# Kernel optimization log

Measured on AMD Instinct MI355X. Metric: run time of the kernel, lower is better.

## Reference

```python
import jax, jax.numpy as jnp
import numpy as np

TAU = 0.4
EPS = 1e-8


def setup_inputs() -> dict:
    key = jax.random.key(0)
    k1, k2 = jax.random.split(key)
    B, N, C, M = 4, 4096, 256, 2048
    l_feat = jax.random.normal(k1, (B, N, C), dtype=jnp.float32)
    g_feat = jax.random.normal(k2, (B, C, M), dtype=jnp.float32)
    return {"l_feat": l_feat, "g_feat": g_feat}


def reference(l_feat, g_feat):
    # l_feat: [B, N, C], g_feat: [B, C, M]
    # cosine similarity over channel dim C (torch CosineSimilarity, dim=2)
    l_norm = jnp.linalg.norm(l_feat, axis=2)          # [B, N]
    g_norm = jnp.linalg.norm(g_feat, axis=1)          # [B, M]
    dot = jnp.einsum('bnc,bcm->bnm', l_feat, g_feat)  # [B, N, M]
    cos_sim = dot / jnp.maximum(l_norm[:, :, None] * g_norm[:, None, :], EPS)
    sim = jnp.exp(cos_sim / TAU)                      # [B, N, M]
    # diag_embed(rowsum) followed by linalg.inv and bmm is exactly
    # row-wise division by the degree (row sum)
    sim = sim / jnp.sum(sim, axis=2, keepdims=True)
    # bmm(sim, g_feat^T): [B,N,M] x [B,M,C] -> [B,N,C]
    g_enh = jnp.einsum('bnm,bcm->bnc', sim, g_feat)
    return l_feat + g_enh
```

## Files before the change

kernel.cpp:

```cpp
#include <hip/hip_runtime.h>

#define B_ 4
#define N_ 4096
#define C_ 256
#define M_ 2048

typedef __attribute__((ext_vector_type(8))) short short8;
typedef __attribute__((ext_vector_type(4))) float f32x4;

union U16x8 { uint4 u4; unsigned short us[8]; short8 s8; };

__device__ __forceinline__ float bf2f(unsigned short h) {
    unsigned int u = ((unsigned int)h) << 16;
    return __builtin_bit_cast(float, u);
}
__device__ __forceinline__ unsigned short f2bf(float f) {
    unsigned int u = __builtin_bit_cast(unsigned int, f);
    u += 0x7FFFu + ((u >> 16) & 1u);
    return (unsigned short)(u >> 16);
}

#define GLB_AS(p) ((const __attribute__((address_space(1))) unsigned int*)(p))
#define LDS_AS(p) ((__attribute__((address_space(3))) unsigned int*)(p))

__global__ __launch_bounds__(256) void k_prep3(const float* __restrict__ g,
                                               unsigned short* __restrict__ gcm,
                                               unsigned short* __restrict__ gmc) {
    __shared__ float4 red4[16][16];
    __shared__ float4 sInv4[16];
    __shared__ unsigned short T[256 * 66];
    const int b = blockIdx.y, m0 = blockIdx.x * 64;
    const int tid = threadIdx.x;
    const int ml2 = tid & 15, cg = tid >> 4;
    const float* gb = g + (size_t)b * C_ * M_ + m0 + ml2 * 4;
    float4 v4[16];
    float4 ss = {0.f, 0.f, 0.f, 0.f};
#pragma unroll
    for (int i = 0; i < 16; ++i) {
        v4[i] = *(const float4*)(gb + (size_t)(cg * 16 + i) * M_);
        ss.x += v4[i].x * v4[i].x; ss.y += v4[i].y * v4[i].y;
        ss.z += v4[i].z * v4[i].z; ss.w += v4[i].w * v4[i].w;
    }
    red4[cg][ml2] = ss;
    __syncthreads();
    if (tid < 16) {
        float4 t = {0.f, 0.f, 0.f, 0.f};
#pragma unroll
        for (int j = 0; j < 16; ++j) {
            float4 r = red4[j][tid];
            t.x += r.x; t.y += r.y; t.z += r.z; t.w += r.w;
        }
        float4 iv;
        iv.x = 1.f / fmaxf(sqrtf(t.x), 1e-8f);
        iv.y = 1.f / fmaxf(sqrtf(t.y), 1e-8f);
        iv.z = 1.f / fmaxf(sqrtf(t.z), 1e-8f);
        iv.w = 1.f / fmaxf(sqrtf(t.w), 1e-8f);
        sInv4[tid] = iv;
    }
    __syncthreads();
    const float4 iv = sInv4[ml2];
    unsigned short* gcmb = gcm + (size_t)b * C_ * M_ + m0 + ml2 * 4;
#pragma unroll
    for (int i = 0; i < 16; ++i) {
        int c = cg * 16 + i;
        uint2 pk;
        pk.x = (unsigned)f2bf(v4[i].x) | ((unsigned)f2bf(v4[i].y) << 16);
        pk.y = (unsigned)f2bf(v4[i].z) | ((unsigned)f2bf(v4[i].w) << 16);
        *(uint2*)(gcmb + (size_t)c * M_) = pk;
        T[c * 66 + ml2 * 4 + 0] = f2bf(v4[i].x * iv.x);
        T[c * 66 + ml2 * 4 + 1] = f2bf(v4[i].y * iv.y);
        T[c * 66 + ml2 * 4 + 2] = f2bf(v4[i].z * iv.z);
        T[c * 66 + ml2 * 4 + 3] = f2bf(v4[i].w * iv.w);
    }
    __syncthreads();
    unsigned short* gmcb = gmc + ((size_t)b * M_ + m0) * C_;
#pragma unroll
    for (int j = 0; j < 8; ++j) {
        int id = j * 256 + tid;
        int mr = id >> 5, cc8 = (id & 31) * 8;
        U16x8 t;
#pragma unroll
        for (int k = 0; k < 8; ++k) t.us[k] = T[(cc8 + k) * 66 + mr];
        *(uint4*)(gmcb + (size_t)mr * C_ + cc8) = t.u4;
    }
}

__global__ __launch_bounds__(256, 2) void k_main(
    const float* __restrict__ l,
    const unsigned short* __restrict__ gcm,
    const unsigned short* __restrict__ gmc,
    float* __restrict__ out)
{
    __shared__ __align__(16) unsigned short sGmc[64 * 256];
    __shared__ __align__(16) unsigned short sGcm[256 * 64];
    __shared__ __align__(16) unsigned short sP[64 * 72];
    __shared__ float sDen[128];

    const int tid = threadIdx.x;
    const int w = tid >> 6;
    const int lane = tid & 63;
    const int l15 = lane & 15;
    const int quad = lane >> 4;
    const int b = blockIdx.y;
    const int row0 = blockIdx.x * 64;
    const int qrow0 = (w & 1) * 32;
    const int kh = w >> 1;

    int goffA[8], goffB[8];
#pragma unroll
    for (int i = 0; i < 8; ++i) {
        int p = (w * 8 + i) * 64 + lane;
        int rA = p >> 5;
        goffA[i] = rA * 256 + (((p & 31) ^ (rA & 31)) << 3);
        int rB = p >> 3;
        goffB[i] = rB * 2048 + (((p & 7) ^ (rB & 7)) << 3);
    }

    const unsigned short* gmc_b = gmc + (size_t)b * M_ * C_;
    const unsigned short* gcm_b = gcm + (size_t)b * C_ * M_;

    auto dmaA = [&](int m0) {
#pragma unroll
        for (int i = 0; i < 8; ++i)
            __builtin_amdgcn_global_load_lds(GLB_AS(gmc_b + (size_t)m0 * 256 + goffA[i]),
                                             LDS_AS(&sGmc[(w * 8 + i) * 512]), 16, 0, 0);
    };
    auto dmaB = [&](int m0) {
#pragma unroll
        for (int i = 0; i < 8; ++i)
            __builtin_amdgcn_global_load_lds(GLB_AS(gcm_b + (size_t)m0 + goffB[i]),
                                             LDS_AS(&sGcm[(w * 8 + i) * 512]), 16, 0, 0);
    };

    dmaA(0);
    dmaB(0);

    short8 qf[2][8];
#pragma unroll
    for (int rt = 0; rt < 2; ++rt) {
        const float* lrow = l + ((size_t)b * N_ + row0 + qrow0 + rt * 16 + l15) * C_;
        U16x8 qt[8];
        float ss = 0.f;
#pragma unroll
        for (int kk = 0; kk < 8; ++kk) {
            float4 x0 = *(const float4*)(lrow + kk * 32 + quad * 8);
            float4 x1 = *(const float4*)(lrow + kk * 32 + quad * 8 + 4);
            ss += x0.x*x0.x + x0.y*x0.y + x0.z*x0.z + x0.w*x0.w;
            ss += x1.x*x1.x + x1.y*x1.y + x1.z*x1.z + x1.w*x1.w;
            qt[kk].us[0] = f2bf(x0.x); qt[kk].us[1] = f2bf(x0.y);
            qt[kk].us[2] = f2bf(x0.z); qt[kk].us[3] = f2bf(x0.w);
            qt[kk].us[4] = f2bf(x1.x); qt[kk].us[5] = f2bf(x1.y);
            qt[kk].us[6] = f2bf(x1.z); qt[kk].us[7] = f2bf(x1.w);
        }
        ss += __shfl_xor(ss, 16);
        ss += __shfl_xor(ss, 32);
        const float invl = 1.0f / fmaxf(sqrtf(ss), 1e-8f);
#pragma unroll
        for (int kk = 0; kk < 8; ++kk) {
            U16x8 t;
#pragma unroll
            for (int j = 0; j < 8; ++j) t.us[j] = f2bf(bf2f(qt[kk].us[j]) * invl);
            qf[rt][kk] = t.s8;
        }
    }

    __syncthreads();

    f32x4 zero = {0.f, 0.f, 0.f, 0.f};
    f32x4 o[4][4];
#pragma unroll
    for (int i = 0; i < 4; ++i)
#pragma unroll
        for (int j = 0; j < 4; ++j) o[i][j] = zero;
    float dl[2][4] = {{0.f,0.f,0.f,0.f},{0.f,0.f,0.f,0.f}};

    for (int mt = 0; mt < 32; ++mt) {
        f32x4 sa[2][2];
        sa[0][0] = zero; sa[0][1] = zero; sa[1][0] = zero; sa[1][1] = zero;
#pragma unroll
        for (int kk = 0; kk < 8; ++kk) {
#pragma unroll
            for (int ct = 0; ct < 2; ++ct) {
                const int row = kh * 32 + ct * 16 + l15;
                const int j = ((kk * 4 + quad) ^ (row & 31)) << 3;
                short8 bb = *(const short8*)&sGmc[row * 256 + j];
                sa[0][ct] = __builtin_amdgcn_mfma_f32_16x16x32_bf16(qf[0][kk], bb, sa[0][ct], 0, 0, 0);
                sa[1][ct] = __builtin_amdgcn_mfma_f32_16x16x32_bf16(qf[1][kk], bb, sa[1][ct], 0, 0, 0);
            }
        }
#pragma unroll
        for (int rt = 0; rt < 2; ++rt)
#pragma unroll
            for (int ct = 0; ct < 2; ++ct)
#pragma unroll
                for (int r = 0; r < 4; ++r) {
                    float p = exp2f(sa[rt][ct][r] * 3.6067376022224085f);
                    dl[rt][r] += p;
                    sP[(qrow0 + rt * 16 + quad * 4 + r) * 72 + kh * 32 + ct * 16 + l15] = f2bf(p);
                }
        __syncthreads();
        if (mt < 31) dmaA((mt + 1) * 64);

#pragma unroll
        for (int k2 = 0; k2 < 2; ++k2) {
            const int off = k2 * 32 + quad * 8;
            short8 a[4];
#pragma unroll
            for (int rt = 0; rt < 4; ++rt)
                a[rt] = *(const short8*)&sP[(rt * 16 + l15) * 72 + off];
#pragma unroll
            for (int ct = 0; ct < 4; ++ct) {
                const int crow = w * 64 + ct * 16 + l15;
                const int j = ((k2 * 4 + quad) ^ (crow & 7)) << 3;
                short8 bb = *(const short8*)&sGcm[crow * 64 + j];
#pragma unroll
                for (int rt = 0; rt < 4; ++rt)
                    o[rt][ct] = __builtin_amdgcn_mfma_f32_16x16x32_bf16(a[rt], bb, o[rt][ct], 0, 0, 0);
            }
        }
        __syncthreads();
        if (mt < 31) dmaB((mt + 1) * 64);
    }

#pragma unroll
    for (int rt = 0; rt < 2; ++rt)
#pragma unroll
        for (int r = 0; r < 4; ++r) {
            float d = dl[rt][r];
            d += __shfl_xor(d, 1);
            d += __shfl_xor(d, 2);
            d += __shfl_xor(d, 4);
            d += __shfl_xor(d, 8);
            if (l15 == 0) sDen[kh * 64 + qrow0 + rt * 16 + quad * 4 + r] = d;
        }
    __syncthreads();

    const float* lb = l + ((size_t)b * N_ + row0) * C_;
    float* ob = out + ((size_t)b * N_ + row0) * C_;
#pragma unroll
    for (int rt = 0; rt < 4; ++rt) {
#pragma unroll
        for (int r = 0; r < 4; ++r) {
            const int row = rt * 16 + quad * 4 + r;
            const float inv = 1.f / (sDen[row] + sDen[64 + row]);
            const size_t rbase = (size_t)row * C_;
#pragma unroll
            for (int ct = 0; ct < 4; ++ct) {
                const int c = w * 64 + ct * 16 + l15;
                ob[rbase + c] = lb[rbase + c] + o[rt][ct][r] * inv;
            }
        }
    }
}

extern "C" void kernel_launch(void* const* d_in, const int* in_sizes, int n_in,
                              void* d_out, int out_size, void* d_ws, size_t ws_size,
                              hipStream_t stream) {
    (void)in_sizes; (void)n_in; (void)out_size; (void)ws_size;
    const float* l = (const float*)d_in[0];
    const float* g = (const float*)d_in[1];
    float* outp = (float*)d_out;

    char* ws = (char*)d_ws;
    unsigned short* gmc = (unsigned short*)ws;
    unsigned short* gcm = (unsigned short*)(ws + (size_t)B_ * M_ * C_ * 2);

    k_prep3<<<dim3(M_ / 64, B_), 256, 0, stream>>>(g, gcm, gmc);
    k_main<<<dim3(N_ / 64, B_), 256, 0, stream>>>(l, gcm, gmc, outp);
}
```

Baseline: 153.5 us.

## Split g preprocessing into norm and cast kernels; halve main kernel row tile

The single preprocessing kernel becomes two: one computes inverse column norms of g, and a second, more parallel kernel casts g to bf16 in both layouts using 64x64 tiles across C. The main kernel now processes 32 query rows per block instead of 64, doubling the grid to 512 blocks so more CUs are busy, with fewer accumulator registers per thread. In exchange, each block reloads the full g tiles for half as many rows, doubling LDS/global traffic per useful MFMA, and an extra kernel launch is added.

```diff
diff --git a/kernel.cpp b/kernel.cpp
--- a/kernel.cpp
+++ b/kernel.cpp
@@ -23,61 +23,59 @@
 #define GLB_AS(p) ((const __attribute__((address_space(1))) unsigned int*)(p))
 #define LDS_AS(p) ((__attribute__((address_space(3))) unsigned int*)(p))
 
-__global__ __launch_bounds__(256) void k_prep3(const float* __restrict__ g,
-                                               unsigned short* __restrict__ gcm,
-                                               unsigned short* __restrict__ gmc) {
-    __shared__ float4 red4[16][16];
-    __shared__ float4 sInv4[16];
-    __shared__ unsigned short T[256 * 66];
+__global__ __launch_bounds__(256) void k_norm(const float* __restrict__ g,
+                                              float* __restrict__ invgn) {
+    __shared__ float red[4][64];
     const int b = blockIdx.y, m0 = blockIdx.x * 64;
     const int tid = threadIdx.x;
-    const int ml2 = tid & 15, cg = tid >> 4;
-    const float* gb = g + (size_t)b * C_ * M_ + m0 + ml2 * 4;
-    float4 v4[16];
-    float4 ss = {0.f, 0.f, 0.f, 0.f};
-#pragma unroll
-    for (int i = 0; i < 16; ++i) {
-        v4[i] = *(const float4*)(gb + (size_t)(cg * 16 + i) * M_);
-        ss.x += v4[i].x * v4[i].x; ss.y += v4[i].y * v4[i].y;
-        ss.z += v4[i].z * v4[i].z; ss.w += v4[i].w * v4[i].w;
-    }
-    red4[cg][ml2] = ss;
-    __syncthreads();
-    if (tid < 16) {
-        float4 t = {0.f, 0.f, 0.f, 0.f};
-#pragma unroll
-        for (int j = 0; j < 16; ++j) {
-            float4 r = red4[j][tid];
-            t.x += r.x; t.y += r.y; t.z += r.z; t.w += r.w;
-        }
-        float4 iv;
-        iv.x = 1.f / fmaxf(sqrtf(t.x), 1e-8f);
-        iv.y = 1.f / fmaxf(sqrtf(t.y), 1e-8f);
-        iv.z = 1.f / fmaxf(sqrtf(t.z), 1e-8f);
-        iv.w = 1.f / fmaxf(sqrtf(t.w), 1e-8f);
-        sInv4[tid] = iv;
-    }
-    __syncthreads();
-    const float4 iv = sInv4[ml2];
-    unsigned short* gcmb = gcm + (size_t)b * C_ * M_ + m0 + ml2 * 4;
-#pragma unroll
-    for (int i = 0; i < 16; ++i) {
-        int c = cg * 16 + i;
+    const int ml = tid & 63, cq = tid >> 6;
+    const float* gb = g + (size_t)b * C_ * M_ + m0 + ml;
+    float ss = 0.f;
+#pragma unroll 8
+    for (int i = 0; i < 64; ++i) {
+        float v = gb[(size_t)(cq * 64 + i) * M_];
+        ss += v * v;
+    }
+    red[cq][ml] = ss;
+    __syncthreads();
+    if (cq == 0) {
+        float t = red[0][ml] + red[1][ml] + red[2][ml] + red[3][ml];
+        invgn[b * M_ + m0 + ml] = 1.f / fmaxf(sqrtf(t), 1e-8f);
+    }
+}
+
+__global__ __launch_bounds__(256) void k_cast(const float* __restrict__ g,
+                                              const float* __restrict__ invgn,
+                                              unsigned short* __restrict__ gcm,
+                                              unsigned short* __restrict__ gmc) {
+    __shared__ unsigned short T[64 * 66];
+    __shared__ float sInv[64];
+    const int b = blockIdx.z, c0 = blockIdx.y * 64, m0 = blockIdx.x * 64;
+    const int tid = threadIdx.x;
+    if (tid < 64) sInv[tid] = invgn[b * M_ + m0 + tid];
+    __syncthreads();
+    const float* gbase = g + ((size_t)b * C_ + c0) * M_ + m0;
+    unsigned short* gcmb = gcm + ((size_t)b * C_ + c0) * M_ + m0;
+#pragma unroll
+    for (int j = 0; j < 4; ++j) {
+        int id = tid + 256 * j;
+        int ci = id >> 4, mq = (id & 15) * 4;
+        float4 v = *(const float4*)(gbase + (size_t)ci * M_ + mq);
         uint2 pk;
-        pk.x = (unsigned)f2bf(v4[i].x) | ((unsigned)f2bf(v4[i].y) << 16);
-        pk.y = (unsigned)f2bf(v4[i].z) | ((unsigned)f2bf(v4[i].w) << 16);
-        *(uint2*)(gcmb + (size_t)c * M_) = pk;
-        T[c * 66 + ml2 * 4 + 0] = f2bf(v4[i].x * iv.x);
-        T[c * 66 + ml2 * 4 + 1] = f2bf(v4[i].y * iv.y);
-        T[c * 66 + ml2 * 4 + 2] = f2bf(v4[i].z * iv.z);
-        T[c * 66 + ml2 * 4 + 3] = f2bf(v4[i].w * iv.w);
-    }
-    __syncthreads();
-    unsigned short* gmcb = gmc + ((size_t)b * M_ + m0) * C_;
-#pragma unroll
-    for (int j = 0; j < 8; ++j) {
-        int id = j * 256 + tid;
-        int mr = id >> 5, cc8 = (id & 31) * 8;
+        pk.x = (unsigned)f2bf(v.x) | ((unsigned)f2bf(v.y) << 16);
+        pk.y = (unsigned)f2bf(v.z) | ((unsigned)f2bf(v.w) << 16);
+        *(uint2*)(gcmb + (size_t)ci * M_ + mq) = pk;
+        T[ci * 66 + mq + 0] = f2bf(v.x * sInv[mq + 0]);
+        T[ci * 66 + mq + 1] = f2bf(v.y * sInv[mq + 1]);
+        T[ci * 66 + mq + 2] = f2bf(v.z * sInv[mq + 2]);
+        T[ci * 66 + mq + 3] = f2bf(v.w * sInv[mq + 3]);
+    }
+    __syncthreads();
+    unsigned short* gmcb = gmc + ((size_t)b * M_ + m0) * C_ + c0;
+#pragma unroll
+    for (int j = 0; j < 2; ++j) {
+        int id = tid + 256 * j;
+        int mr = id >> 3, cc8 = (id & 7) * 8;
         U16x8 t;
 #pragma unroll
         for (int k = 0; k < 8; ++k) t.us[k] = T[(cc8 + k) * 66 + mr];
@@ -93,8 +91,8 @@
 {
     __shared__ __align__(16) unsigned short sGmc[64 * 256];
     __shared__ __align__(16) unsigned short sGcm[256 * 64];
-    __shared__ __align__(16) unsigned short sP[64 * 72];
-    __shared__ float sDen[128];
+    __shared__ __align__(16) unsigned short sP[32 * 72];
+    __shared__ float sDen[2][32];
 
     const int tid = threadIdx.x;
     const int w = tid >> 6;
@@ -102,8 +100,8 @@
     const int l15 = lane & 15;
     const int quad = lane >> 4;
     const int b = blockIdx.y;
-    const int row0 = blockIdx.x * 64;
-    const int qrow0 = (w & 1) * 32;
+    const int row0 = blockIdx.x * 32;
+    const int rh = (w & 1) * 16;
     const int kh = w >> 1;
 
     int goffA[8], goffB[8];
@@ -135,48 +133,45 @@
     dmaA(0);
     dmaB(0);
 
-    short8 qf[2][8];
-#pragma unroll
-    for (int rt = 0; rt < 2; ++rt) {
-        const float* lrow = l + ((size_t)b * N_ + row0 + qrow0 + rt * 16 + l15) * C_;
-        U16x8 qt[8];
-        float ss = 0.f;
-#pragma unroll
-        for (int kk = 0; kk < 8; ++kk) {
-            float4 x0 = *(const float4*)(lrow + kk * 32 + quad * 8);
-            float4 x1 = *(const float4*)(lrow + kk * 32 + quad * 8 + 4);
-            ss += x0.x*x0.x + x0.y*x0.y + x0.z*x0.z + x0.w*x0.w;
-            ss += x1.x*x1.x + x1.y*x1.y + x1.z*x1.z + x1.w*x1.w;
-            qt[kk].us[0] = f2bf(x0.x); qt[kk].us[1] = f2bf(x0.y);
-            qt[kk].us[2] = f2bf(x0.z); qt[kk].us[3] = f2bf(x0.w);
-            qt[kk].us[4] = f2bf(x1.x); qt[kk].us[5] = f2bf(x1.y);
-            qt[kk].us[6] = f2bf(x1.z); qt[kk].us[7] = f2bf(x1.w);
-        }
-        ss += __shfl_xor(ss, 16);
-        ss += __shfl_xor(ss, 32);
-        const float invl = 1.0f / fmaxf(sqrtf(ss), 1e-8f);
-#pragma unroll
-        for (int kk = 0; kk < 8; ++kk) {
-            U16x8 t;
-#pragma unroll
-            for (int j = 0; j < 8; ++j) t.us[j] = f2bf(bf2f(qt[kk].us[j]) * invl);
-            qf[rt][kk] = t.s8;
-        }
+    const float* lrow = l + ((size_t)b * N_ + row0 + rh + l15) * C_;
+    U16x8 qt[8];
+    float ss = 0.f;
+#pragma unroll
+    for (int kk = 0; kk < 8; ++kk) {
+        float4 x0 = *(const float4*)(lrow + kk * 32 + quad * 8);
+        float4 x1 = *(const float4*)(lrow + kk * 32 + quad * 8 + 4);
+        ss += x0.x*x0.x + x0.y*x0.y + x0.z*x0.z + x0.w*x0.w;
+        ss += x1.x*x1.x + x1.y*x1.y + x1.z*x1.z + x1.w*x1.w;
+        qt[kk].us[0] = f2bf(x0.x); qt[kk].us[1] = f2bf(x0.y);
+        qt[kk].us[2] = f2bf(x0.z); qt[kk].us[3] = f2bf(x0.w);
+        qt[kk].us[4] = f2bf(x1.x); qt[kk].us[5] = f2bf(x1.y);
+        qt[kk].us[6] = f2bf(x1.z); qt[kk].us[7] = f2bf(x1.w);
+    }
+    ss += __shfl_xor(ss, 16);
+    ss += __shfl_xor(ss, 32);
+    const float invl = 1.0f / fmaxf(sqrtf(ss), 1e-8f);
+    short8 qf[8];
+#pragma unroll
+    for (int kk = 0; kk < 8; ++kk) {
+        U16x8 t;
+#pragma unroll
+        for (int j = 0; j < 8; ++j) t.us[j] = f2bf(bf2f(qt[kk].us[j]) * invl);
+        qf[kk] = t.s8;
     }
 
     __syncthreads();
 
     f32x4 zero = {0.f, 0.f, 0.f, 0.f};
-    f32x4 o[4][4];
-#pragma unroll
-    for (int i = 0; i < 4; ++i)
+    f32x4 o[2][4];
+#pragma unroll
+    for (int i = 0; i < 2; ++i)
 #pragma unroll
         for (int j = 0; j < 4; ++j) o[i][j] = zero;
-    float dl[2][4] = {{0.f,0.f,0.f,0.f},{0.f,0.f,0.f,0.f}};
+    float dl[4] = {0.f, 0.f, 0.f, 0.f};
 
     for (int mt = 0; mt < 32; ++mt) {
-        f32x4 sa[2][2];
-        sa[0][0] = zero; sa[0][1] = zero; sa[1][0] = zero; sa[1][1] = zero;
+        f32x4 sa[2];
+        sa[0] = zero; sa[1] = zero;
 #pragma unroll
         for (int kk = 0; kk < 8; ++kk) {
 #pragma unroll
@@ -184,29 +179,26 @@
                 const int row = kh * 32 + ct * 16 + l15;
                 const int j = ((kk * 4 + quad) ^ (row & 31)) << 3;
                 short8 bb = *(const short8*)&sGmc[row * 256 + j];
-                sa[0][ct] = __builtin_amdgcn_mfma_f32_16x16x32_bf16(qf[0][kk], bb, sa[0][ct], 0, 0, 0);
-                sa[1][ct] = __builtin_amdgcn_mfma_f32_16x16x32_bf16(qf[1][kk], bb, sa[1][ct], 0, 0, 0);
+                sa[ct] = __builtin_amdgcn_mfma_f32_16x16x32_bf16(qf[kk], bb, sa[ct], 0, 0, 0);
             }
         }
 #pragma unroll
-        for (int rt = 0; rt < 2; ++rt)
-#pragma unroll
-            for (int ct = 0; ct < 2; ++ct)
-#pragma unroll
-                for (int r = 0; r < 4; ++r) {
-                    float p = exp2f(sa[rt][ct][r] * 3.6067376022224085f);
-                    dl[rt][r] += p;
-                    sP[(qrow0 + rt * 16 + quad * 4 + r) * 72 + kh * 32 + ct * 16 + l15] = f2bf(p);
-                }
+        for (int ct = 0; ct < 2; ++ct)
+#pragma unroll
+            for (int r = 0; r < 4; ++r) {
+                float p = exp2f(sa[ct][r] * 3.6067376022224085f);
+                dl[r] += p;
+                sP[(rh + quad * 4 + r) * 72 + kh * 32 + ct * 16 + l15] = f2bf(p);
+            }
         __syncthreads();
         if (mt < 31) dmaA((mt + 1) * 64);
 
 #pragma unroll
         for (int k2 = 0; k2 < 2; ++k2) {
             const int off = k2 * 32 + quad * 8;
-            short8 a[4];
-#pragma unroll
-            for (int rt = 0; rt < 4; ++rt)
+            short8 a[2];
+#pragma unroll
+            for (int rt = 0; rt < 2; ++rt)
                 a[rt] = *(const short8*)&sP[(rt * 16 + l15) * 72 + off];
 #pragma unroll
             for (int ct = 0; ct < 4; ++ct) {
@@ -214,7 +206,7 @@
                 const int j = ((k2 * 4 + quad) ^ (crow & 7)) << 3;
                 short8 bb = *(const short8*)&sGcm[crow * 64 + j];
 #pragma unroll
-                for (int rt = 0; rt < 4; ++rt)
+                for (int rt = 0; rt < 2; ++rt)
                     o[rt][ct] = __builtin_amdgcn_mfma_f32_16x16x32_bf16(a[rt], bb, o[rt][ct], 0, 0, 0);
             }
         }
@@ -223,26 +215,24 @@
     }
 
 #pragma unroll
-    for (int rt = 0; rt < 2; ++rt)
-#pragma unroll
-        for (int r = 0; r < 4; ++r) {
-            float d = dl[rt][r];
-            d += __shfl_xor(d, 1);
-            d += __shfl_xor(d, 2);
-            d += __shfl_xor(d, 4);
-            d += __shfl_xor(d, 8);
-            if (l15 == 0) sDen[kh * 64 + qrow0 + rt * 16 + quad * 4 + r] = d;
-        }
+    for (int r = 0; r < 4; ++r) {
+        float d = dl[r];
+        d += __shfl_xor(d, 1);
+        d += __shfl_xor(d, 2);
+        d += __shfl_xor(d, 4);
+        d += __shfl_xor(d, 8);
+        if (l15 == 0) sDen[kh][rh + quad * 4 + r] = d;
+    }
     __syncthreads();
 
     const float* lb = l + ((size_t)b * N_ + row0) * C_;
     float* ob = out + ((size_t)b * N_ + row0) * C_;
 #pragma unroll
-    for (int rt = 0; rt < 4; ++rt) {
+    for (int rt = 0; rt < 2; ++rt) {
 #pragma unroll
         for (int r = 0; r < 4; ++r) {
             const int row = rt * 16 + quad * 4 + r;
-            const float inv = 1.f / (sDen[row] + sDen[64 + row]);
+            const float inv = 1.f / (sDen[0][row] + sDen[1][row]);
             const size_t rbase = (size_t)row * C_;
 #pragma unroll
             for (int ct = 0; ct < 4; ++ct) {
@@ -264,7 +254,9 @@
     char* ws = (char*)d_ws;
     unsigned short* gmc = (unsigned short*)ws;
     unsigned short* gcm = (unsigned short*)(ws + (size_t)B_ * M_ * C_ * 2);
-
-    k_prep3<<<dim3(M_ / 64, B_), 256, 0, stream>>>(g, gcm, gmc);
-    k_main<<<dim3(N_ / 64, B_), 256, 0, stream>>>(l, gcm, gmc, outp);
-}
+    float* invgn = (float*)(ws + 2 * (size_t)B_ * M_ * C_ * 2);
+
+    k_norm<<<dim3(M_ / 64, B_), 256, 0, stream>>>(g, invgn);
+    k_cast<<<dim3(M_ / 64, C_ / 64, B_), 256, 0, stream>>>(g, invgn, gcm, gmc);
+    k_main<<<dim3(N_ / 32, B_), 256, 0, stream>>>(l, gcm, gmc, outp);
+}
```

New measurement: 142.4 us. 1.08x faster.
